# Kernel optimization log

Hardware: AMD Instinct MI355X
Metric: run time of the kernel (lower is better)

## Reference

```python
import jax, jax.numpy as jnp
import numpy as np

B, S, D = 8, 1024, 1024
H, K = 16, 64  # num_heads, key_dim
NEG_INF = -1e9  # Keras _large_compatible_negative for float32


def setup_inputs() -> dict:
    key = jax.random.key(0)
    ks = jax.random.split(key, 10)
    x = jax.random.normal(ks[0], (B, S, D), dtype=jnp.float32)
    mask = jax.random.bernoulli(ks[1], 0.9, (B, S))  # bool per-token mask
    w = lambda k, shp: (0.02 * jax.random.normal(k, shp, dtype=jnp.float32))
    return {
        "input_tensor": x,
        "input_mask": mask,
        "Wq": w(ks[2], (D, H, K)), "bq": jnp.zeros((H, K), jnp.float32),
        "Wk": w(ks[3], (D, H, K)), "bk": jnp.zeros((H, K), jnp.float32),
        "Wv": w(ks[4], (D, H, K)), "bv": jnp.zeros((H, K), jnp.float32),
        "Wo": w(ks[5], (H, K, D)), "bo": jnp.zeros((D,), jnp.float32),
    }


def reference(input_tensor, input_mask, Wq, bq, Wk, bk, Wv, bv, Wo, bo):
    x = input_tensor
    # QKV projections: [B,S,D] x [D,H,K] -> [B,S,H,K]
    q = jnp.einsum("bsd,dhk->bshk", x, Wq) + bq
    k = jnp.einsum("bsd,dhk->bshk", x, Wk) + bk
    v = jnp.einsum("bsd,dhk->bshk", x, Wv) + bv
    # scaled dot-product scores: [B,H,Sq,Sk]
    scores = jnp.einsum("bqhk,bshk->bhqs", q, k) / jnp.sqrt(
        jnp.asarray(K, x.dtype))
    # mask = logical_and(mask[...,None], mask[...,None,:]) per example
    m2 = (input_mask[:, :, None] & input_mask[:, None, :])  # [B,Sq,Sk]
    scores = scores + (1.0 - m2[:, None, :, :].astype(x.dtype)) * NEG_INF
    probs = jax.nn.softmax(scores, axis=-1)
    # attend and project out: [B,S,H,K] -> [B,S,D]
    ctx = jnp.einsum("bhqs,bshk->bqhk", probs, v)
    return jnp.einsum("bqhk,hkd->bqd", ctx, Wo) + bo
```

## Files before the change

### kernel.cpp

```cpp
#include <hip/hip_runtime.h>
#include <math.h>

#define Ss 1024
#define Dd 1024
#define Hh 16
#define Kk 64

typedef __bf16 bf16x8 __attribute__((ext_vector_type(8)));
typedef __bf16 bf16x4 __attribute__((ext_vector_type(4)));
typedef float  f32x4  __attribute__((ext_vector_type(4)));

#define MFMA16(a, b, c) __builtin_amdgcn_mfma_f32_16x16x32_bf16(a, b, c, 0, 0, 0)

#define XB_E   8388608u
#define WT_E   3145728u
#define WOT_E  1048576u
#define QKV_E  8388608u

__device__ __forceinline__ float exp2_hw(float x) {
    float r; asm("v_exp_f32 %0, %1" : "=v"(r) : "v"(x)); return r;
}

typedef __attribute__((address_space(1))) const void gas_void;
typedef __attribute__((address_space(3))) void las_void;
__device__ __forceinline__ void gll16(const __bf16* g, char* l) {
    __builtin_amdgcn_global_load_lds((gas_void*)g, (las_void*)l, 16, 0, 0);
}

__global__ __launch_bounds__(256) void prep(
    const float* __restrict__ x,
    const float* __restrict__ Wq, const float* __restrict__ Wk,
    const float* __restrict__ Wv, const float* __restrict__ Wo,
    __bf16* __restrict__ xb, __bf16* __restrict__ WT, __bf16* __restrict__ WoT)
{
    __shared__ float tile[64][65];
    const int z = blockIdx.z;
    const int t = threadIdx.x;

    if (z == 4) {
        size_t blk = blockIdx.y * 16 + blockIdx.x;
        const float4* src = (const float4*)(x + blk * 32768);
        bf16x4* dst = (bf16x4*)(((__bf16*)xb) + blk * 32768);
        #pragma unroll
        for (int u = 0; u < 32; ++u) {
            float4 v = src[u * 256 + t];
            dst[u * 256 + t] =
                (bf16x4){(__bf16)v.x, (__bf16)v.y, (__bf16)v.z, (__bf16)v.w};
        }
        return;
    }

    const float* src = (z == 0) ? Wq : (z == 1) ? Wk : (z == 2) ? Wv : Wo;
    __bf16* dst = (z < 3) ? (WT + (size_t)z * 1048576) : WoT;

    int r0 = blockIdx.y * 64, c0 = blockIdx.x * 64;
    int rr = t >> 2, cg = (t & 3) * 16;

    #pragma unroll
    for (int u = 0; u < 4; ++u) {
        float4 v = *(const float4*)(src + (size_t)(r0 + rr) * 1024 + c0 + cg + u * 4);
        tile[rr][cg + u * 4 + 0] = v.x;
        tile[rr][cg + u * 4 + 1] = v.y;
        tile[rr][cg + u * 4 + 2] = v.z;
        tile[rr][cg + u * 4 + 3] = v.w;
    }
    __syncthreads();
    bf16x8 o0, o1;
    #pragma unroll
    for (int jj = 0; jj < 8; ++jj) o0[jj] = (__bf16)tile[cg + jj][rr];
    #pragma unroll
    for (int jj = 0; jj < 8; ++jj) o1[jj] = (__bf16)tile[cg + 8 + jj][rr];
    __bf16* dp = dst + (size_t)(c0 + rr) * 1024 + r0 + cg;
    *(bf16x8*)dp = o0;
    *(bf16x8*)(dp + 8) = o1;
}

__global__ __launch_bounds__(512, 2) void gemm_bt(
    const __bf16* __restrict__ A, const __bf16* __restrict__ Bt, int mode,
    __bf16* __restrict__ qb, __bf16* __restrict__ kb, __bf16* __restrict__ vb,
    const float* __restrict__ bq, const float* __restrict__ bk,
    const float* __restrict__ bv,
    float* __restrict__ outf, const float* __restrict__ bo)
{
    __shared__ __align__(16) __bf16 As[2][256][64];
    __shared__ __align__(16) __bf16 Bs[2][256][64];

    const int t = threadIdx.x;
    const int wave = t >> 6, lane = t & 63;
    const int quad = lane >> 4, l16 = lane & 15;
    const int wm = wave >> 2, wn = wave & 3;

    const int nwg = gridDim.x * gridDim.y;
    const int cpx = nwg >> 3;
    int g = blockIdx.y * gridDim.x + blockIdx.x;
    g = (g & 7) * cpx + (g >> 3);
    const int bx = g % gridDim.x, by = g / gridDim.x;
    const int m0 = by * 256, n0 = bx * 256;

    const int srow = t >> 3;
    const int scol = (((t & 7) ^ (srow & 7)) * 8);
    const __bf16* pa = A  + (size_t)(m0 + srow) * 1024 + scol;
    const __bf16* pb = Bt + (size_t)(n0 + srow) * 1024 + scol;
    char* lA = (char*)(&As[0][0][0]) + t * 16;
    char* lB = (char*)(&Bs[0][0][0]) + t * 16;

#define STAGE(slot, k0) do {                                     \
        gll16(pa + (k0),           lA + (slot) * 32768);         \
        gll16(pa + (k0) +  65536,  lA + (slot) * 32768 +  8192); \
        gll16(pa + (k0) + 131072,  lA + (slot) * 32768 + 16384); \
        gll16(pa + (k0) + 196608,  lA + (slot) * 32768 + 24576); \
        gll16(pb + (k0),           lB + (slot) * 32768);         \
        gll16(pb + (k0) +  65536,  lB + (slot) * 32768 +  8192); \
        gll16(pb + (k0) + 131072,  lB + (slot) * 32768 + 16384); \
        gll16(pb + (k0) + 196608,  lB + (slot) * 32768 + 24576); \
    } while (0)

    STAGE(0, 0);
    STAGE(1, 64);

    f32x4 acc[8][4];
    #pragma unroll
    for (int i = 0; i < 8; ++i)
        #pragma unroll
        for (int j = 0; j < 4; ++j) acc[i][j] = (f32x4){0.f, 0.f, 0.f, 0.f};

    const int swz = (l16 & 7) << 4;

    for (int it = 0; it < 16; ++it) {
        const int s = it & 1;
        if (it == 15) asm volatile("s_waitcnt vmcnt(0)" ::: "memory");
        else          asm volatile("s_waitcnt vmcnt(8)" ::: "memory");
        __builtin_amdgcn_s_barrier();

        const char* baseA = (const char*)&As[s][0][0];
        const char* baseB = (const char*)&Bs[s][0][0];

        bf16x8 bfrag[2][4];
        #pragma unroll
        for (int nj = 0; nj < 4; ++nj) {
            int rowb = (wn * 64 + nj * 16 + l16) * 128;
            bfrag[0][nj] = *(const bf16x8*)(baseB + rowb + ((quad * 16) ^ swz));
            bfrag[1][nj] = *(const bf16x8*)(baseB + rowb + ((64 + quad * 16) ^ swz));
        }

        {
            bf16x8 afr[4][2];
            #pragma unroll
            for (int mi = 0; mi < 4; ++mi) {
                int rowa = (wm * 128 + mi * 16 + l16) * 128;
                afr[mi][0] = *(const bf16x8*)(baseA + rowa + ((quad * 16) ^ swz));
                afr[mi][1] = *(const bf16x8*)(baseA + rowa + ((64 + quad * 16) ^ swz));
            }
            __builtin_amdgcn_s_setprio(1);
            #pragma unroll
            for (int mi = 0; mi < 4; ++mi)
                #pragma unroll
                for (int nj = 0; nj < 4; ++nj)
                    acc[mi][nj] = MFMA16(afr[mi][1], bfrag[1][nj],
                                  MFMA16(afr[mi][0], bfrag[0][nj], acc[mi][nj]));
            __builtin_amdgcn_s_setprio(0);
        }
        __builtin_amdgcn_s_barrier();

        {
            bf16x8 afr[4][2];
            #pragma unroll
            for (int mi = 0; mi < 4; ++mi) {
                int rowa = (wm * 128 + (mi + 4) * 16 + l16) * 128;
                afr[mi][0] = *(const bf16x8*)(baseA + rowa + ((quad * 16) ^ swz));
                afr[mi][1] = *(const bf16x8*)(baseA + rowa + ((64 + quad * 16) ^ swz));
            }
            asm volatile("s_waitcnt lgkmcnt(0)" ::: "memory");
            __builtin_amdgcn_sched_barrier(0);
            __builtin_amdgcn_s_barrier();
            if (it < 14) STAGE(s, (it + 2) * 64);

            __builtin_amdgcn_s_setprio(1);
            #pragma unroll
            for (int mi = 0; mi < 4; ++mi)
                #pragma unroll
                for (int nj = 0; nj < 4; ++nj)
                    acc[mi + 4][nj] = MFMA16(afr[mi][1], bfrag[1][nj],
                                      MFMA16(afr[mi][0], bfrag[0][nj], acc[mi + 4][nj]));
            __builtin_amdgcn_s_setprio(0);
        }
    }
#undef STAGE

    if (mode == 0) {
        const int z = n0 >> 10;
        const float* bias = (z == 0) ? bq : (z == 1) ? bk : bv;
        const float sc2 = (z == 0) ? 0.18033688011112042f : 1.0f;
        #pragma unroll
        for (int mi = 0; mi < 8; ++mi) {
            int row = m0 + wm * 128 + mi * 16 + quad * 4;
            int b = row >> 10, sx = row & 1023;
            #pragma unroll
            for (int nj = 0; nj < 4; ++nj) {
                int n1 = (n0 + wn * 64 + nj * 16 + l16) & 1023;
                int h = n1 >> 6, ch = n1 & 63;
                float bia = bias[n1];
                if (z < 2) {
                    __bf16* dst = ((z == 0) ? qb : kb)
                        + ((size_t)(b * Hh + h) * Ss + sx) * Kk + ch;
                    #pragma unroll
                    for (int r = 0; r < 4; ++r)
                        dst[(size_t)r * Kk] = (__bf16)((acc[mi][nj][r] + bia) * sc2);
                } else {
                    bf16x4 o;
                    #pragma unroll
                    for (int r = 0; r < 4; ++r) o[r] = (__bf16)(acc[mi][nj][r] + bia);
                    *(bf16x4*)(vb + ((size_t)(b * Hh + h) * Kk + ch) * Ss + sx) = o;
                }
            }
        }
    } else {
        #pragma unroll
        for (int mi = 0; mi < 8; ++mi) {
            int row = m0 + wm * 128 + mi * 16 + quad * 4;
            #pragma unroll
            for (int nj = 0; nj < 4; ++nj) {
                int n = n0 + wn * 64 + nj * 16 + l16;
                float bia = bo[n];
                #pragma unroll
                for (int r = 0; r < 4; ++r)
                    outf[(size_t)(row + r) * 1024 + n] = acc[mi][nj][r] + bia;
            }
        }
    }
}

__global__ __launch_bounds__(256) void attn(
    const __bf16* __restrict__ qb, const __bf16* __restrict__ kb,
    const __bf16* __restrict__ vb, const int* __restrict__ mask,
    __bf16* __restrict__ ctx)
{
    const int bh = blockIdx.x;
    const int q0 = blockIdx.y * 128;
    const int b  = bh >> 4;
    const int h  = bh & 15;
    const size_t base = (size_t)bh * Ss * Kk;

    __shared__ __align__(16) __bf16 Qs[128][72];
    __shared__ __align__(16) __bf16 Ks[2][64][72];
    __shared__ __align__(16) __bf16 VTs[2][64][72];
    __shared__ __align__(16) __bf16 Ps[4][32][72];
    __shared__ float mkf[1024];

    const int t    = threadIdx.x;
    const int wave = t >> 6, lane = t & 63;
    const int quad = lane >> 4, l16 = lane & 15;
    const int qbase = wave * 32;

    #pragma unroll
    for (int p = 0; p < 4; ++p) {
        int idx = t + p * 256;
        int r = idx >> 3, g = idx & 7;
        *(bf16x8*)&Qs[r][g * 8] =
            *(const bf16x8*)(qb + base + (size_t)(q0 + r) * Kk + g * 8);
    }
    {
        int4 mi = *(const int4*)(mask + b * Ss + t * 4);
        mkf[t * 4 + 0] = (float)mi.x;
        mkf[t * 4 + 1] = (float)mi.y;
        mkf[t * 4 + 2] = (float)mi.z;
        mkf[t * 4 + 3] = (float)mi.w;
    }

    const int r0 = t >> 3, c0 = (t & 7) * 8;
    bf16x8 kr0, kr1, vr0, vr1;
    kr0 = *(const bf16x8*)(kb + base + (size_t)(r0) * Kk + c0);
    kr1 = *(const bf16x8*)(kb + base + (size_t)(r0 + 32) * Kk + c0);
    vr0 = *(const bf16x8*)(vb + base + (size_t)(r0) * Ss + c0);
    vr1 = *(const bf16x8*)(vb + base + (size_t)(r0 + 32) * Ss + c0);

    __syncthreads();

    bf16x8 aq[2][2];
    #pragma unroll
    for (int rg = 0; rg < 2; ++rg) {
        aq[rg][0] = *(const bf16x8*)&Qs[qbase + rg * 16 + l16][quad * 8];
        aq[rg][1] = *(const bf16x8*)&Qs[qbase + rg * 16 + l16][32 + quad * 8];
    }
    float mqf[2][4], omqf[2][4];
    #pragma unroll
    for (int rg = 0; rg < 2; ++rg)
        #pragma unroll
        for (int i = 0; i < 4; ++i) {
            float m = mkf[q0 + qbase + rg * 16 + quad * 4 + i];
            mqf[rg][i] = m; omqf[rg][i] = 1.0f - m;
        }

    f32x4 O[2][4];
    float lsum[2][4];
    #pragma unroll
    for (int rg = 0; rg < 2; ++rg)
        #pragma unroll
        for (int nb = 0; nb < 4; ++nb) O[rg][nb] = (f32x4){0.f, 0.f, 0.f, 0.f};
    #pragma unroll
    for (int rg = 0; rg < 2; ++rg)
        #pragma unroll
        for (int i = 0; i < 4; ++i) lsum[rg][i] = 0.f;

    for (int kt = 0; kt < Ss; kt += 64) {
        const int p = (kt >> 6) & 1;
        *(bf16x8*)&Ks[p][r0][c0] = kr0;
        *(bf16x8*)&Ks[p][r0 + 32][c0] = kr1;
        *(bf16x8*)&VTs[p][r0][c0] = vr0;
        *(bf16x8*)&VTs[p][r0 + 32][c0] = vr1;
        __syncthreads();

        int ktn = kt + 64;
        if (ktn < Ss) {
            kr0 = *(const bf16x8*)(kb + base + (size_t)(ktn + r0) * Kk + c0);
            kr1 = *(const bf16x8*)(kb + base + (size_t)(ktn + r0 + 32) * Kk + c0);
            vr0 = *(const bf16x8*)(vb + base + (size_t)(r0) * Ss + ktn + c0);
            vr1 = *(const bf16x8*)(vb + base + (size_t)(r0 + 32) * Ss + ktn + c0);
        }

        float mkv[4];
        #pragma unroll
        for (int nb = 0; nb < 4; ++nb) mkv[nb] = mkf[kt + nb * 16 + l16];

        bf16x8 kb0[4], kb1[4];
        #pragma unroll
        for (int nb = 0; nb < 4; ++nb) {
            kb0[nb] = *(const bf16x8*)&Ks[p][nb * 16 + l16][quad * 8];
            kb1[nb] = *(const bf16x8*)&Ks[p][nb * 16 + l16][32 + quad * 8];
        }

        f32x4 s[2][4];
        __builtin_amdgcn_s_setprio(1);
        #pragma unroll
        for (int rg = 0; rg < 2; ++rg)
            #pragma unroll
            for (int nb = 0; nb < 4; ++nb) {
                f32x4 a = (f32x4){0.f, 0.f, 0.f, 0.f};
                a = MFMA16(aq[rg][0], kb0[nb], a);
                a = MFMA16(aq[rg][1], kb1[nb], a);
                s[rg][nb] = a;
            }
        __builtin_amdgcn_s_setprio(0);

        #pragma unroll
        for (int rg = 0; rg < 2; ++rg)
            #pragma unroll
            for (int i = 0; i < 4; ++i) {
                float ls = 0.f;
                #pragma unroll
                for (int nb = 0; nb < 4; ++nb) {
                    float pv = exp2_hw(s[rg][nb][i]) * mkv[nb];
                    pv = pv * mqf[rg][i] + omqf[rg][i];
                    Ps[wave][rg * 16 + quad * 4 + i][nb * 16 + l16] = (__bf16)pv;
                    ls += pv;
                }
                lsum[rg][i] += ls;
            }

        bf16x8 ap0[2], ap1[2];
        #pragma unroll
        for (int rg = 0; rg < 2; ++rg) {
            ap0[rg] = *(const bf16x8*)&Ps[wave][rg * 16 + l16][quad * 8];
            ap1[rg] = *(const bf16x8*)&Ps[wave][rg * 16 + l16][32 + quad * 8];
        }
        __builtin_amdgcn_s_setprio(1);
        #pragma unroll
        for (int nb = 0; nb < 4; ++nb) {
            bf16x8 vb0 = *(const bf16x8*)&VTs[p][nb * 16 + l16][quad * 8];
            bf16x8 vb1 = *(const bf16x8*)&VTs[p][nb * 16 + l16][32 + quad * 8];
            #pragma unroll
            for (int rg = 0; rg < 2; ++rg) {
                O[rg][nb] = MFMA16(ap0[rg], vb0, O[rg][nb]);
                O[rg][nb] = MFMA16(ap1[rg], vb1, O[rg][nb]);
            }
        }
        __builtin_amdgcn_s_setprio(0);
    }

    #pragma unroll
    for (int rg = 0; rg < 2; ++rg)
        #pragma unroll
        for (int i = 0; i < 4; ++i) {
            float l = lsum[rg][i];
            l += __shfl_xor(l, 1);
            l += __shfl_xor(l, 2);
            l += __shfl_xor(l, 4);
            l += __shfl_xor(l, 8);
            float inv = 1.0f / l;
            int srow = q0 + qbase + rg * 16 + quad * 4 + i;
            __bf16* dst = ctx + ((size_t)(b * Ss + srow) * Hh + h) * Kk;
            #pragma unroll
            for (int nb = 0; nb < 4; ++nb)
                dst[nb * 16 + l16] = (__bf16)(O[rg][nb][i] * inv);
        }
}

extern "C" void kernel_launch(void* const* d_in, const int* in_sizes, int n_in,
                              void* d_out, int out_size, void* d_ws, size_t ws_size,
                              hipStream_t stream) {
    const float* x    = (const float*)d_in[0];
    const int*   mask = (const int*)d_in[1];
    const float* Wq   = (const float*)d_in[2];
    const float* bq   = (const float*)d_in[3];
    const float* Wk   = (const float*)d_in[4];
    const float* bk   = (const float*)d_in[5];
    const float* Wv   = (const float*)d_in[6];
    const float* bv   = (const float*)d_in[7];
    const float* Wo   = (const float*)d_in[8];
    const float* bo   = (const float*)d_in[9];

    __bf16* xb   = (__bf16*)d_ws;
    __bf16* WT   = xb + XB_E;
    __bf16* WoT  = WT + WT_E;
    __bf16* qb   = WoT + WOT_E;
    __bf16* kb   = qb + QKV_E;
    __bf16* vb   = kb + QKV_E;
    __bf16* ctxb = vb + QKV_E;
    float* out = (float*)d_out;

    prep<<<dim3(16, 16, 5), 256, 0, stream>>>(x, Wq, Wk, Wv, Wo, xb, WT, WoT);
    gemm_bt<<<dim3(12, 32), 512, 0, stream>>>(xb, WT, 0, qb, kb, vb,
                                              bq, bk, bv, nullptr, nullptr);
    attn<<<dim3(128, 8), 256, 0, stream>>>(qb, kb, vb, mask, ctxb);
    gemm_bt<<<dim3(4, 32), 512, 0, stream>>>(ctxb, WoT, 1, nullptr, nullptr,
                                             nullptr, nullptr, nullptr, nullptr,
                                             out, bo);
}
```

Measured before the change: 266.6 us.

## Template GEMM on N-tile width so both projections launch 256 workgroups

The GEMM kernel becomes a template on the N tile width. The QKV projection uses 256x384 tiles and the output projection uses 256x128 tiles, so each launches exactly 256 workgroups (8x32 grid) to fill the CUs evenly instead of 384 and 128. The pipeline changes from prefetching two stages ahead to one stage ahead with a full vmcnt(0) wait each iteration, and B fragments are now loaded in halves to limit register pressure. The QKV epilogue now picks q, k or v per 16-column group, since a tile can straddle those boundaries. Risks are more exposed load latency from the shallower prefetch and higher register use from the wider accumulators.

```diff
diff --git a/kernel.cpp b/kernel.cpp
--- a/kernel.cpp
+++ b/kernel.cpp
@@ -16,6 +16,8 @@
 #define WT_E   3145728u
 #define WOT_E  1048576u
 #define QKV_E  8388608u
+
+#define QSC 0.18033688011112042f
 
 __device__ __forceinline__ float exp2_hw(float x) {
     float r; asm("v_exp_f32 %0, %1" : "=v"(r) : "v"(x)); return r;
@@ -75,27 +77,30 @@
     *(bf16x8*)(dp + 8) = o1;
 }
 
-__global__ __launch_bounds__(512, 2) void gemm_bt(
+template <int BN>
+__global__ __launch_bounds__(512) void gemm_bt(
     const __bf16* __restrict__ A, const __bf16* __restrict__ Bt, int mode,
     __bf16* __restrict__ qb, __bf16* __restrict__ kb, __bf16* __restrict__ vb,
     const float* __restrict__ bq, const float* __restrict__ bk,
     const float* __restrict__ bv,
     float* __restrict__ outf, const float* __restrict__ bo)
 {
+    constexpr int NJ  = BN / 64;
+    constexpr int NJH = NJ / 2;
+    constexpr int WN  = BN / 4;
+
     __shared__ __align__(16) __bf16 As[2][256][64];
-    __shared__ __align__(16) __bf16 Bs[2][256][64];
+    __shared__ __align__(16) __bf16 Bs[2][BN][64];
 
     const int t = threadIdx.x;
     const int wave = t >> 6, lane = t & 63;
     const int quad = lane >> 4, l16 = lane & 15;
     const int wm = wave >> 2, wn = wave & 3;
 
-    const int nwg = gridDim.x * gridDim.y;
-    const int cpx = nwg >> 3;
     int g = blockIdx.y * gridDim.x + blockIdx.x;
-    g = (g & 7) * cpx + (g >> 3);
+    g = (g & 7) * 32 + (g >> 3);
     const int bx = g % gridDim.x, by = g / gridDim.x;
-    const int m0 = by * 256, n0 = bx * 256;
+    const int m0 = by * 256, n0 = bx * BN;
 
     const int srow = t >> 3;
     const int scol = (((t & 7) ^ (srow & 7)) * 8);
@@ -104,109 +109,93 @@
     char* lA = (char*)(&As[0][0][0]) + t * 16;
     char* lB = (char*)(&Bs[0][0][0]) + t * 16;
 
-#define STAGE(slot, k0) do {                                     \
-        gll16(pa + (k0),           lA + (slot) * 32768);         \
-        gll16(pa + (k0) +  65536,  lA + (slot) * 32768 +  8192); \
-        gll16(pa + (k0) + 131072,  lA + (slot) * 32768 + 16384); \
-        gll16(pa + (k0) + 196608,  lA + (slot) * 32768 + 24576); \
-        gll16(pb + (k0),           lB + (slot) * 32768);         \
-        gll16(pb + (k0) +  65536,  lB + (slot) * 32768 +  8192); \
-        gll16(pb + (k0) + 131072,  lB + (slot) * 32768 + 16384); \
-        gll16(pb + (k0) + 196608,  lB + (slot) * 32768 + 24576); \
+#define STAGE(slot, k0) do {                                                  \
+        _Pragma("unroll")                                                     \
+        for (int g_ = 0; g_ < 4; ++g_)                                        \
+            gll16(pa + (k0) + g_ * 65536, lA + (slot) * 32768 + g_ * 8192);   \
+        _Pragma("unroll")                                                     \
+        for (int g_ = 0; g_ < BN / 64; ++g_)                                  \
+            gll16(pb + (k0) + g_ * 65536, lB + (slot) * (BN * 128) + g_ * 8192); \
     } while (0)
 
     STAGE(0, 0);
-    STAGE(1, 64);
-
-    f32x4 acc[8][4];
+
+    f32x4 acc[8][NJ];
     #pragma unroll
     for (int i = 0; i < 8; ++i)
         #pragma unroll
-        for (int j = 0; j < 4; ++j) acc[i][j] = (f32x4){0.f, 0.f, 0.f, 0.f};
+        for (int j = 0; j < NJ; ++j) acc[i][j] = (f32x4){0.f, 0.f, 0.f, 0.f};
 
     const int swz = (l16 & 7) << 4;
 
     for (int it = 0; it < 16; ++it) {
         const int s = it & 1;
-        if (it == 15) asm volatile("s_waitcnt vmcnt(0)" ::: "memory");
-        else          asm volatile("s_waitcnt vmcnt(8)" ::: "memory");
+        asm volatile("s_waitcnt vmcnt(0)" ::: "memory");
         __builtin_amdgcn_s_barrier();
+        if (it < 15) STAGE(s ^ 1, (it + 1) * 64);
 
         const char* baseA = (const char*)&As[s][0][0];
         const char* baseB = (const char*)&Bs[s][0][0];
 
-        bf16x8 bfrag[2][4];
-        #pragma unroll
-        for (int nj = 0; nj < 4; ++nj) {
-            int rowb = (wn * 64 + nj * 16 + l16) * 128;
-            bfrag[0][nj] = *(const bf16x8*)(baseB + rowb + ((quad * 16) ^ swz));
-            bfrag[1][nj] = *(const bf16x8*)(baseB + rowb + ((64 + quad * 16) ^ swz));
-        }
-
-        {
+        #pragma unroll
+        for (int mh = 0; mh < 2; ++mh) {
             bf16x8 afr[4][2];
             #pragma unroll
             for (int mi = 0; mi < 4; ++mi) {
-                int rowa = (wm * 128 + mi * 16 + l16) * 128;
+                int rowa = (wm * 128 + (mh * 4 + mi) * 16 + l16) * 128;
                 afr[mi][0] = *(const bf16x8*)(baseA + rowa + ((quad * 16) ^ swz));
                 afr[mi][1] = *(const bf16x8*)(baseA + rowa + ((64 + quad * 16) ^ swz));
             }
-            __builtin_amdgcn_s_setprio(1);
-            #pragma unroll
-            for (int mi = 0; mi < 4; ++mi)
+            #pragma unroll
+            for (int nh = 0; nh < 2; ++nh) {
+                bf16x8 bfr[NJH][2];
                 #pragma unroll
-                for (int nj = 0; nj < 4; ++nj)
-                    acc[mi][nj] = MFMA16(afr[mi][1], bfrag[1][nj],
-                                  MFMA16(afr[mi][0], bfrag[0][nj], acc[mi][nj]));
-            __builtin_amdgcn_s_setprio(0);
-        }
-        __builtin_amdgcn_s_barrier();
-
-        {
-            bf16x8 afr[4][2];
-            #pragma unroll
-            for (int mi = 0; mi < 4; ++mi) {
-                int rowa = (wm * 128 + (mi + 4) * 16 + l16) * 128;
-                afr[mi][0] = *(const bf16x8*)(baseA + rowa + ((quad * 16) ^ swz));
-                afr[mi][1] = *(const bf16x8*)(baseA + rowa + ((64 + quad * 16) ^ swz));
-            }
-            asm volatile("s_waitcnt lgkmcnt(0)" ::: "memory");
-            __builtin_amdgcn_sched_barrier(0);
-            __builtin_amdgcn_s_barrier();
-            if (it < 14) STAGE(s, (it + 2) * 64);
-
-            __builtin_amdgcn_s_setprio(1);
-            #pragma unroll
-            for (int mi = 0; mi < 4; ++mi)
+                for (int nj = 0; nj < NJH; ++nj) {
+                    int rowb = (wn * WN + (nh * NJH + nj) * 16 + l16) * 128;
+                    bfr[nj][0] = *(const bf16x8*)(baseB + rowb + ((quad * 16) ^ swz));
+                    bfr[nj][1] = *(const bf16x8*)(baseB + rowb + ((64 + quad * 16) ^ swz));
+                }
+                __builtin_amdgcn_s_setprio(1);
                 #pragma unroll
-                for (int nj = 0; nj < 4; ++nj)
-                    acc[mi + 4][nj] = MFMA16(afr[mi][1], bfrag[1][nj],
-                                      MFMA16(afr[mi][0], bfrag[0][nj], acc[mi + 4][nj]));
-            __builtin_amdgcn_s_setprio(0);
+                for (int mi = 0; mi < 4; ++mi)
+                    #pragma unroll
+                    for (int nj = 0; nj < NJH; ++nj)
+                        acc[mh * 4 + mi][nh * NJH + nj] =
+                            MFMA16(afr[mi][1], bfr[nj][1],
+                            MFMA16(afr[mi][0], bfr[nj][0],
+                                   acc[mh * 4 + mi][nh * NJH + nj]));
+                __builtin_amdgcn_s_setprio(0);
+            }
+            if (mh == 0) __builtin_amdgcn_s_barrier();
         }
     }
 #undef STAGE
 
     if (mode == 0) {
-        const int z = n0 >> 10;
-        const float* bias = (z == 0) ? bq : (z == 1) ? bk : bv;
-        const float sc2 = (z == 0) ? 0.18033688011112042f : 1.0f;
         #pragma unroll
         for (int mi = 0; mi < 8; ++mi) {
             int row = m0 + wm * 128 + mi * 16 + quad * 4;
             int b = row >> 10, sx = row & 1023;
             #pragma unroll
-            for (int nj = 0; nj < 4; ++nj) {
-                int n1 = (n0 + wn * 64 + nj * 16 + l16) & 1023;
+            for (int nj = 0; nj < NJ; ++nj) {
+                int c16 = n0 + wn * WN + nj * 16;
+                int z = c16 >> 10;
+                int n1 = (c16 + l16) & 1023;
                 int h = n1 >> 6, ch = n1 & 63;
-                float bia = bias[n1];
-                if (z < 2) {
-                    __bf16* dst = ((z == 0) ? qb : kb)
-                        + ((size_t)(b * Hh + h) * Ss + sx) * Kk + ch;
+                if (z == 0) {
+                    float bia = bq[n1];
+                    __bf16* dst = qb + ((size_t)(b * Hh + h) * Ss + sx) * Kk + ch;
                     #pragma unroll
                     for (int r = 0; r < 4; ++r)
-                        dst[(size_t)r * Kk] = (__bf16)((acc[mi][nj][r] + bia) * sc2);
+                        dst[(size_t)r * Kk] = (__bf16)((acc[mi][nj][r] + bia) * QSC);
+                } else if (z == 1) {
+                    float bia = bk[n1];
+                    __bf16* dst = kb + ((size_t)(b * Hh + h) * Ss + sx) * Kk + ch;
+                    #pragma unroll
+                    for (int r = 0; r < 4; ++r)
+                        dst[(size_t)r * Kk] = (__bf16)(acc[mi][nj][r] + bia);
                 } else {
+                    float bia = bv[n1];
                     bf16x4 o;
                     #pragma unroll
                     for (int r = 0; r < 4; ++r) o[r] = (__bf16)(acc[mi][nj][r] + bia);
@@ -219,8 +208,8 @@
         for (int mi = 0; mi < 8; ++mi) {
             int row = m0 + wm * 128 + mi * 16 + quad * 4;
             #pragma unroll
-            for (int nj = 0; nj < 4; ++nj) {
-                int n = n0 + wn * 64 + nj * 16 + l16;
+            for (int nj = 0; nj < NJ; ++nj) {
+                int n = n0 + wn * WN + nj * 16 + l16;
                 float bia = bo[n];
                 #pragma unroll
                 for (int r = 0; r < 4; ++r)
@@ -419,10 +408,10 @@
     float* out = (float*)d_out;
 
     prep<<<dim3(16, 16, 5), 256, 0, stream>>>(x, Wq, Wk, Wv, Wo, xb, WT, WoT);
-    gemm_bt<<<dim3(12, 32), 512, 0, stream>>>(xb, WT, 0, qb, kb, vb,
-                                              bq, bk, bv, nullptr, nullptr);
+    gemm_bt<384><<<dim3(8, 32), 512, 0, stream>>>(xb, WT, 0, qb, kb, vb,
+                                                  bq, bk, bv, nullptr, nullptr);
     attn<<<dim3(128, 8), 256, 0, stream>>>(qb, kb, vb, mask, ctxb);
-    gemm_bt<<<dim3(4, 32), 512, 0, stream>>>(ctxb, WoT, 1, nullptr, nullptr,
-                                             nullptr, nullptr, nullptr, nullptr,
-                                             out, bo);
-}
+    gemm_bt<128><<<dim3(8, 32), 512, 0, stream>>>(ctxb, WoT, 1, nullptr, nullptr,
+                                                  nullptr, nullptr, nullptr,
+                                                  nullptr, out, bo);
+}
```

After: 266.6 us. No clear change (+0.0%).

## Split output GEMM into narrower-tile kernel and remap attention block order

Applied to the files above, without the earlier changes.

The output projection gets its own kernel with 256x128 tiles, which doubles the grid from 128 to 256 workgroups so the device's compute units are better filled for the small N=1024 GEMM. The new kernel has its own double-buffered direct-to-LDS load schedule. The attention grid index is also remapped so consecutive blocks go to different (batch, head) pairs, spreading K/V reuse across the XCDs. The risks are lower data reuse per tile and a more complex pipeline in the new kernel.

```diff
diff --git a/kernel.cpp b/kernel.cpp
--- a/kernel.cpp
+++ b/kernel.cpp
@@ -16,6 +16,8 @@
 #define WT_E   3145728u
 #define WOT_E  1048576u
 #define QKV_E  8388608u
+
+#define QSC 0.18033688011112042f
 
 __device__ __forceinline__ float exp2_hw(float x) {
     float r; asm("v_exp_f32 %0, %1" : "=v"(r) : "v"(x)); return r;
@@ -75,12 +77,11 @@
     *(bf16x8*)(dp + 8) = o1;
 }
 
-__global__ __launch_bounds__(512, 2) void gemm_bt(
-    const __bf16* __restrict__ A, const __bf16* __restrict__ Bt, int mode,
+__global__ __launch_bounds__(512, 2) void gemm_qkv(
+    const __bf16* __restrict__ A, const __bf16* __restrict__ Bt,
     __bf16* __restrict__ qb, __bf16* __restrict__ kb, __bf16* __restrict__ vb,
     const float* __restrict__ bq, const float* __restrict__ bk,
-    const float* __restrict__ bv,
-    float* __restrict__ outf, const float* __restrict__ bo)
+    const float* __restrict__ bv)
 {
     __shared__ __align__(16) __bf16 As[2][256][64];
     __shared__ __align__(16) __bf16 Bs[2][256][64];
@@ -187,10 +188,10 @@
     }
 #undef STAGE
 
-    if (mode == 0) {
+    {
         const int z = n0 >> 10;
         const float* bias = (z == 0) ? bq : (z == 1) ? bk : bv;
-        const float sc2 = (z == 0) ? 0.18033688011112042f : 1.0f;
+        const float sc2 = (z == 0) ? QSC : 1.0f;
         #pragma unroll
         for (int mi = 0; mi < 8; ++mi) {
             int row = m0 + wm * 128 + mi * 16 + quad * 4;
@@ -207,25 +208,131 @@
                     for (int r = 0; r < 4; ++r)
                         dst[(size_t)r * Kk] = (__bf16)((acc[mi][nj][r] + bia) * sc2);
                 } else {
+                    float bia2 = bv[n1];
                     bf16x4 o;
                     #pragma unroll
-                    for (int r = 0; r < 4; ++r) o[r] = (__bf16)(acc[mi][nj][r] + bia);
+                    for (int r = 0; r < 4; ++r) o[r] = (__bf16)(acc[mi][nj][r] + bia2);
                     *(bf16x4*)(vb + ((size_t)(b * Hh + h) * Kk + ch) * Ss + sx) = o;
                 }
             }
         }
-    } else {
-        #pragma unroll
-        for (int mi = 0; mi < 8; ++mi) {
-            int row = m0 + wm * 128 + mi * 16 + quad * 4;
-            #pragma unroll
-            for (int nj = 0; nj < 4; ++nj) {
-                int n = n0 + wn * 64 + nj * 16 + l16;
-                float bia = bo[n];
-                #pragma unroll
-                for (int r = 0; r < 4; ++r)
-                    outf[(size_t)(row + r) * 1024 + n] = acc[mi][nj][r] + bia;
-            }
+    }
+}
+
+__global__ __launch_bounds__(512) void gemm_out(
+    const __bf16* __restrict__ A, const __bf16* __restrict__ Bt,
+    float* __restrict__ outf, const float* __restrict__ bo)
+{
+    __shared__ __align__(16) __bf16 As[2][256][64];
+    __shared__ __align__(16) __bf16 Bs[2][128][64];
+
+    const int t = threadIdx.x;
+    const int wave = t >> 6, lane = t & 63;
+    const int quad = lane >> 4, l16 = lane & 15;
+    const int wm = wave >> 2, wn = wave & 3;
+
+    const int nwg = gridDim.x * gridDim.y;
+    const int cpx = nwg >> 3;
+    int g = blockIdx.y * gridDim.x + blockIdx.x;
+    g = (g & 7) * cpx + (g >> 3);
+    const int bx = g % gridDim.x, by = g / gridDim.x;
+    const int m0 = by * 256, n0 = bx * 128;
+
+    const int srow = t >> 3;
+    const int scol = (((t & 7) ^ (srow & 7)) * 8);
+    const __bf16* pa = A  + (size_t)(m0 + srow) * 1024 + scol;
+    const __bf16* pb = Bt + (size_t)(n0 + srow) * 1024 + scol;
+    char* lA = (char*)(&As[0][0][0]) + t * 16;
+    char* lB = (char*)(&Bs[0][0][0]) + t * 16;
+
+#define SGA(slot, k0, c) gll16(pa + (k0) + (c) * 65536, lA + (slot) * 32768 + (c) * 8192)
+#define SGB(slot, k0, c) gll16(pb + (k0) + (c) * 65536, lB + (slot) * 16384 + (c) * 8192)
+
+    SGA(0, 0, 0); SGA(0, 0, 2);
+    SGB(0, 0, 0); SGB(0, 0, 1);
+    SGA(0, 0, 1); SGA(0, 0, 3);
+
+    f32x4 acc[8][2];
+    #pragma unroll
+    for (int i = 0; i < 8; ++i)
+        #pragma unroll
+        for (int j = 0; j < 2; ++j) acc[i][j] = (f32x4){0.f, 0.f, 0.f, 0.f};
+
+    const int swz = (l16 & 7) << 4;
+
+    asm volatile("s_waitcnt vmcnt(2)" ::: "memory");
+    __syncthreads();
+
+    for (int it = 0; it < 16; ++it) {
+        const int s = it & 1, ns = s ^ 1;
+        const int kn = (it + 1) * 64;
+        const bool st = (it < 15);
+        const char* baseA = (const char*)&As[s][0][0];
+        const char* baseB = (const char*)&Bs[s][0][0];
+
+        bf16x8 af[4][2], b0f[2][2];
+
+        asm volatile("s_waitcnt vmcnt(0)" ::: "memory");
+        #pragma unroll
+        for (int mi = 0; mi < 4; ++mi) {
+            int ra = (wm * 128 + mi * 16 + l16) * 128;
+            af[mi][0] = *(const bf16x8*)(baseA + ra + ((quad * 16) ^ swz));
+            af[mi][1] = *(const bf16x8*)(baseA + ra + ((64 + quad * 16) ^ swz));
+        }
+        #pragma unroll
+        for (int nj = 0; nj < 2; ++nj) {
+            int rb = (wn * 32 + nj * 16 + l16) * 128;
+            b0f[nj][0] = *(const bf16x8*)(baseB + rb + ((quad * 16) ^ swz));
+            b0f[nj][1] = *(const bf16x8*)(baseB + rb + ((64 + quad * 16) ^ swz));
+        }
+        if (st) { SGA(ns, kn, 0); SGA(ns, kn, 2); SGB(ns, kn, 0); SGB(ns, kn, 1); }
+        __builtin_amdgcn_s_barrier();
+        asm volatile("s_waitcnt lgkmcnt(0)" ::: "memory");
+        __builtin_amdgcn_sched_barrier(0);
+        __builtin_amdgcn_s_setprio(1);
+        #pragma unroll
+        for (int mi = 0; mi < 4; ++mi)
+            #pragma unroll
+            for (int nj = 0; nj < 2; ++nj)
+                acc[mi][nj] = MFMA16(af[mi][1], b0f[nj][1],
+                              MFMA16(af[mi][0], b0f[nj][0], acc[mi][nj]));
+        __builtin_amdgcn_s_setprio(0);
+        __builtin_amdgcn_s_barrier();
+
+        asm volatile("s_waitcnt vmcnt(0)" ::: "memory");
+        #pragma unroll
+        for (int mi = 0; mi < 4; ++mi) {
+            int ra = (wm * 128 + (4 + mi) * 16 + l16) * 128;
+            af[mi][0] = *(const bf16x8*)(baseA + ra + ((quad * 16) ^ swz));
+            af[mi][1] = *(const bf16x8*)(baseA + ra + ((64 + quad * 16) ^ swz));
+        }
+        if (st) { SGA(ns, kn, 1); SGA(ns, kn, 3); }
+        __builtin_amdgcn_s_barrier();
+        asm volatile("s_waitcnt lgkmcnt(0)" ::: "memory");
+        __builtin_amdgcn_sched_barrier(0);
+        __builtin_amdgcn_s_setprio(1);
+        #pragma unroll
+        for (int mi = 0; mi < 4; ++mi)
+            #pragma unroll
+            for (int nj = 0; nj < 2; ++nj)
+                acc[4 + mi][nj] = MFMA16(af[mi][1], b0f[nj][1],
+                                  MFMA16(af[mi][0], b0f[nj][0], acc[4 + mi][nj]));
+        __builtin_amdgcn_s_setprio(0);
+        __builtin_amdgcn_s_barrier();
+    }
+#undef SGA
+#undef SGB
+
+    #pragma unroll
+    for (int mi = 0; mi < 8; ++mi) {
+        int row = m0 + wm * 128 + mi * 16 + quad * 4;
+        #pragma unroll
+        for (int nj = 0; nj < 2; ++nj) {
+            int n = n0 + wn * 32 + nj * 16 + l16;
+            float bia = bo[n];
+            #pragma unroll
+            for (int r = 0; r < 4; ++r)
+                outf[(size_t)(row + r) * 1024 + n] = acc[mi][nj][r] + bia;
         }
     }
 }
@@ -235,8 +342,9 @@
     const __bf16* __restrict__ vb, const int* __restrict__ mask,
     __bf16* __restrict__ ctx)
 {
-    const int bh = blockIdx.x;
-    const int q0 = blockIdx.y * 128;
+    const int id = blockIdx.y * gridDim.x + blockIdx.x;
+    const int bh = (id & 7) * 16 + ((id >> 3) & 15);
+    const int q0 = (id >> 7) * 128;
     const int b  = bh >> 4;
     const int h  = bh & 15;
     const size_t base = (size_t)bh * Ss * Kk;
@@ -255,9 +363,9 @@
     #pragma unroll
     for (int p = 0; p < 4; ++p) {
         int idx = t + p * 256;
-        int r = idx >> 3, g = idx & 7;
-        *(bf16x8*)&Qs[r][g * 8] =
-            *(const bf16x8*)(qb + base + (size_t)(q0 + r) * Kk + g * 8);
+        int r = idx >> 3, gq = idx & 7;
+        *(bf16x8*)&Qs[r][gq * 8] =
+            *(const bf16x8*)(qb + base + (size_t)(q0 + r) * Kk + gq * 8);
     }
     {
         int4 mi = *(const int4*)(mask + b * Ss + t * 4);
@@ -419,10 +527,7 @@
     float* out = (float*)d_out;
 
     prep<<<dim3(16, 16, 5), 256, 0, stream>>>(x, Wq, Wk, Wv, Wo, xb, WT, WoT);
-    gemm_bt<<<dim3(12, 32), 512, 0, stream>>>(xb, WT, 0, qb, kb, vb,
-                                              bq, bk, bv, nullptr, nullptr);
+    gemm_qkv<<<dim3(12, 32), 512, 0, stream>>>(xb, WT, qb, kb, vb, bq, bk, bv);
     attn<<<dim3(128, 8), 256, 0, stream>>>(qb, kb, vb, mask, ctxb);
-    gemm_bt<<<dim3(4, 32), 512, 0, stream>>>(ctxb, WoT, 1, nullptr, nullptr,
-                                             nullptr, nullptr, nullptr, nullptr,
-                                             out, bo);
-}
+    gemm_out<<<dim3(8, 32), 512, 0, stream>>>(ctxb, WoT, out, bo);
+}
```

Measured after the change: 259.8 us. -2.5%, faster.
